# Kernel optimization log

Measured on AMD Instinct MI355X. Metric: run time of the kernel, lower is better.

Reference implementation:

```python
import jax, jax.numpy as jnp
import numpy as np

D_MODEL, D_STATE, D_CONV, EXPAND, DT_RANK = 1024, 16, 4, 2, 64
D_INNER = EXPAND * D_MODEL


def setup_inputs() -> dict:
    key = jax.random.key(0)
    ks = jax.random.split(key, 10)
    B, L = 2, 2048
    x = jax.random.normal(ks[0], (B, L, D_MODEL), dtype=jnp.float32)
    # torch nn.Linear weights are [out, in]; applied as x @ W.T
    in_proj_w = jax.random.normal(ks[1], (2 * D_INNER, D_MODEL), jnp.float32) * (D_MODEL ** -0.5)
    conv_w = jax.random.normal(ks[2], (D_INNER, 1, D_CONV), jnp.float32) * (D_CONV ** -0.5)
    conv_b = jax.random.normal(ks[3], (D_INNER,), jnp.float32) * 0.01
    x_proj_w = jax.random.normal(ks[4], (DT_RANK + 2 * D_STATE, D_INNER), jnp.float32) * (D_INNER ** -0.5)
    dt_init_std = DT_RANK ** -0.5
    dt_proj_w = jax.random.uniform(ks[5], (D_INNER, DT_RANK), jnp.float32, -dt_init_std, dt_init_std)
    # dt bias init: inverse-softplus of dt ~ LogUniform(1e-3, 1e-1)
    dt = jnp.exp(jax.random.uniform(ks[6], (D_INNER,), jnp.float32) * (np.log(0.1) - np.log(0.001)) + np.log(0.001))
    dt_proj_b = dt + jnp.log(-jnp.expm1(-dt))
    A_log = jnp.log(jnp.tile(jnp.arange(1, D_STATE + 1, dtype=jnp.float32), (D_INNER, 1)))  # [D_INNER, N]
    D_skip = jnp.ones((D_INNER,), jnp.float32)
    out_proj_w = jax.random.normal(ks[7], (D_MODEL, D_INNER), jnp.float32) * (D_INNER ** -0.5)
    return {"x": x, "in_proj_w": in_proj_w, "conv_w": conv_w, "conv_b": conv_b,
            "x_proj_w": x_proj_w, "dt_proj_w": dt_proj_w, "dt_proj_b": dt_proj_b,
            "A_log": A_log, "D_skip": D_skip, "out_proj_w": out_proj_w}


def selective_scan(u, delta, A, Bmat, Cmat, D_skip):
    # u, delta: [B, L, D]; A: [D, N]; Bmat, Cmat: [B, L, N]; D_skip: [D]
    def step(h, inp):
        delta_t, B_t, C_t, u_t = inp  # [B,D], [B,N], [B,N], [B,D]
        dA = jnp.exp(delta_t[..., None] * A)                      # [B,D,N]
        h = dA * h + (delta_t * u_t)[..., None] * B_t[:, None, :]  # [B,D,N]
        y_t = jnp.einsum('bdn,bn->bd', h, C_t)
        return h, y_t
    B_size, L, D_size = u.shape
    h0 = jnp.zeros((B_size, D_size, A.shape[-1]), u.dtype)
    xs = (jnp.swapaxes(delta, 0, 1), jnp.swapaxes(Bmat, 0, 1),
          jnp.swapaxes(Cmat, 0, 1), jnp.swapaxes(u, 0, 1))
    _, ys = jax.lax.scan(step, h0, xs)          # ys: [L, B, D]
    y = jnp.swapaxes(ys, 0, 1)                  # [B, L, D]
    return y + u * D_skip


def reference(x, in_proj_w, conv_w, conv_b, x_proj_w, dt_proj_w, dt_proj_b, A_log, D_skip, out_proj_w):
    B_size, L, _ = x.shape
    xz = x @ in_proj_w.T                         # [B, L, 2*D_INNER]
    x_ssm, z = jnp.split(xz, 2, axis=-1)
    # causal depthwise conv1d (torch pads d_conv-1 both sides then takes [:L])
    x_c = jnp.swapaxes(x_ssm, 1, 2)              # [B, D_INNER, L]
    x_c = jax.lax.conv_general_dilated(
        x_c, conv_w, window_strides=(1,), padding=[(D_CONV - 1, 0)],
        dimension_numbers=('NCH', 'OIH', 'NCH'), feature_group_count=D_INNER)
    x_c = x_c + conv_b[None, :, None]
    x_ssm = jax.nn.silu(jnp.swapaxes(x_c, 1, 2))  # [B, L, D_INNER]
    x_dbl = x_ssm @ x_proj_w.T                    # [B, L, dt_rank + 2N]
    dt, Bm, Cm = jnp.split(x_dbl, [DT_RANK, DT_RANK + D_STATE], axis=-1)
    delta = jax.nn.softplus(dt @ dt_proj_w.T + dt_proj_b)  # [B, L, D_INNER]
    A = -jnp.exp(A_log)                           # [D_INNER, N]
    y = selective_scan(x_ssm, delta, A, Bm, Cm, D_skip)
    y = y * jax.nn.silu(z)
    return y @ out_proj_w.T                       # [B, L, d_model]
```

## Files before the change

### kernel.cpp

```cpp
#include <hip/hip_runtime.h>
#include <hip/hip_bf16.h>
#include <math.h>

#define NB      2
#define LSEQ    2048
#define BLTOK   4096
#define DM      1024
#define DI      2048
#define NST     16
#define DTR     64
#define CH      64
#define LC      32

typedef __attribute__((ext_vector_type(8))) short short8;
typedef __attribute__((ext_vector_type(4))) float f32x4;

#define LDS_PTR(p) ((__attribute__((address_space(3))) void*)(p))
#define GLB_PTR(p) ((const __attribute__((address_space(1))) void*)(p))

static __device__ __forceinline__ unsigned short f2bf(float f) {
    unsigned int u = __float_as_uint(f);
    unsigned int r = (u + 0x7FFFu + ((u >> 16) & 1u)) >> 16;
    return (unsigned short)r;
}
static __device__ __forceinline__ float bf2f(unsigned short v) {
    return __uint_as_float((unsigned int)v << 16);
}

__launch_bounds__(256)
__global__ void cast_bf16(const float* __restrict__ in, unsigned short* __restrict__ out, int n4)
{
    int i = blockIdx.x * 256 + threadIdx.x;
    if (i < n4) {
        float4 v = ((const float4*)in)[i];
        uint2 o;
        o.x = (unsigned)f2bf(v.x) | ((unsigned)f2bf(v.y) << 16);
        o.y = (unsigned)f2bf(v.z) | ((unsigned)f2bf(v.w) << 16);
        ((uint2*)out)[i] = o;
    }
}

template<int EPI>
__launch_bounds__(256)
__global__ void gemm_db(const unsigned short* __restrict__ A,
                        const unsigned short* __restrict__ W,
                        void* __restrict__ Cout,
                        const float* __restrict__ bias,
                        int M, int N, int K, int lda, int ldb, int ldc)
{
    __shared__ unsigned short lds[2][2][128 * 64];

    const int tid = threadIdx.x;
    const int l = tid & 63;
    const int w = tid >> 6;
    const int wr = w >> 1, wc = w & 1;
    const int brow = blockIdx.y * 128;
    const int bcol = blockIdx.x * 128;

    const int strow = tid >> 3;
    const int scol  = ((tid & 7) ^ (strow & 7)) * 8;

    f32x4 acc[4][4];
#pragma unroll
    for (int i = 0; i < 4; ++i)
#pragma unroll
        for (int j = 0; j < 4; ++j) acc[i][j] = (f32x4)0.f;

    auto stage = [&](int bb, int k0) {
#pragma unroll
        for (int i = 0; i < 4; ++i) {
            const unsigned short* ga = A + (size_t)(brow + i * 32 + strow) * lda + k0 + scol;
            __builtin_amdgcn_global_load_lds(GLB_PTR(ga),
                LDS_PTR((char*)&lds[bb][0][0] + (i * 32 + w * 8) * 128), 16, 0, 0);
            const unsigned short* gb = W + (size_t)(bcol + i * 32 + strow) * ldb + k0 + scol;
            __builtin_amdgcn_global_load_lds(GLB_PTR(gb),
                LDS_PTR((char*)&lds[bb][1][0] + (i * 32 + w * 8) * 128), 16, 0, 0);
        }
    };

    auto compute = [&](int bb) {
        const char* baseA = (const char*)&lds[bb][0][0];
        const char* baseB = (const char*)&lds[bb][1][0];
        const int xo  = (l & 7) * 16;
        const int ko0 = (l >> 4) * 16;
#pragma unroll
        for (int ks = 0; ks < 2; ++ks) {
            const int kb = ks * 64 + ko0;
            short8 af[4], bfr[4];
#pragma unroll
            for (int i = 0; i < 4; ++i) {
                const int rowA = wr * 64 + i * 16 + (l & 15);
                af[i] = *(const short8*)(baseA + rowA * 128 + (kb ^ xo));
                const int rowB = wc * 64 + i * 16 + (l & 15);
                bfr[i] = *(const short8*)(baseB + rowB * 128 + (kb ^ xo));
            }
#pragma unroll
            for (int i = 0; i < 4; ++i)
#pragma unroll
                for (int j = 0; j < 4; ++j)
                    acc[i][j] = __builtin_amdgcn_mfma_f32_16x16x32_bf16(af[i], bfr[j], acc[i][j], 0, 0, 0);
        }
    };

    const int nt = K / 64;
    stage(0, 0);
    __syncthreads();
    int cur = 0;
    for (int t = 0; t < nt - 1; ++t) {
        stage(cur ^ 1, (t + 1) * 64);
        compute(cur);
        __syncthreads();
        cur ^= 1;
    }
    compute(cur);

#pragma unroll
    for (int i = 0; i < 4; ++i) {
        const int row0 = brow + wr * 64 + i * 16 + ((l >> 4) * 4);
#pragma unroll
        for (int j = 0; j < 4; ++j) {
            const int col = bcol + wc * 64 + j * 16 + (l & 15);
            if (EPI == 1) {
                unsigned short* Cb = (unsigned short*)Cout;
#pragma unroll
                for (int r = 0; r < 4; ++r)
                    Cb[(size_t)(row0 + r) * ldc + col] = f2bf(acc[i][j][r]);
            } else if (EPI == 2) {
                float* Cf = (float*)Cout;
                const float bv = bias[col];
#pragma unroll
                for (int r = 0; r < 4; ++r) {
                    float v = acc[i][j][r] + bv;
                    Cf[(size_t)(row0 + r) * ldc + col] = (v > 20.f) ? v : log1pf(__expf(v));
                }
            } else {
                float* Cf = (float*)Cout;
#pragma unroll
                for (int r = 0; r < 4; ++r)
                    Cf[(size_t)(row0 + r) * ldc + col] = acc[i][j][r];
            }
        }
    }
}

__launch_bounds__(256)
__global__ void gemm_mfma_sk(const unsigned short* __restrict__ A,
                             const unsigned short* __restrict__ W,
                             float* __restrict__ Cpart,
                             int M, int N, int K, int lda, int ldb, int ldc, int kslices)
{
    __shared__ unsigned short Asub[128 * 32];
    __shared__ unsigned short Bsub[128 * 32];

    const int tid = threadIdx.x;
    const int l = tid & 63;
    const int w = tid >> 6;
    const int wr = w >> 1, wc = w & 1;
    const int brow = blockIdx.y * 128;
    const int bcol = blockIdx.x * 128;
    const int ks = blockIdx.z;
    const int klen = K / kslices;
    const int kbeg = ks * klen;
    float* C = Cpart + (size_t)ks * M * ldc;

    f32x4 acc[4][4];
#pragma unroll
    for (int i = 0; i < 4; ++i)
#pragma unroll
        for (int j = 0; j < 4; ++j) acc[i][j] = (f32x4)0.f;

    const int srow = tid >> 2;
    const int scol = (tid & 3) * 8;

    for (int k0 = kbeg; k0 < kbeg + klen; k0 += 32) {
#pragma unroll
        for (int i = 0; i < 2; ++i) {
            const int ar = brow + i * 64 + srow;
            const unsigned short* ga = A + (size_t)ar * lda + k0 + scol;
            __builtin_amdgcn_global_load_lds(GLB_PTR(ga),
                LDS_PTR((char*)Asub + i * 4096 + w * 1024), 16, 0, 0);
            int nr = bcol + i * 64 + srow;
            if (nr > N - 1) nr = N - 1;
            const unsigned short* gb = W + (size_t)nr * ldb + k0 + scol;
            __builtin_amdgcn_global_load_lds(GLB_PTR(gb),
                LDS_PTR((char*)Bsub + i * 4096 + w * 1024), 16, 0, 0);
        }
        __syncthreads();

        short8 af[4], bf[4];
#pragma unroll
        for (int i = 0; i < 4; ++i) {
            const int row = wr * 64 + i * 16 + (l & 15);
            af[i] = *(const short8*)((const char*)Asub + row * 64 + (l >> 4) * 16);
        }
#pragma unroll
        for (int j = 0; j < 4; ++j) {
            const int row = wc * 64 + j * 16 + (l & 15);
            bf[j] = *(const short8*)((const char*)Bsub + row * 64 + (l >> 4) * 16);
        }
#pragma unroll
        for (int i = 0; i < 4; ++i)
#pragma unroll
            for (int j = 0; j < 4; ++j)
                acc[i][j] = __builtin_amdgcn_mfma_f32_16x16x32_bf16(af[i], bf[j], acc[i][j], 0, 0, 0);
        __syncthreads();
    }

#pragma unroll
    for (int i = 0; i < 4; ++i) {
        const int row0 = brow + wr * 64 + i * 16 + ((l >> 4) * 4);
#pragma unroll
        for (int j = 0; j < 4; ++j) {
            const int col = bcol + wc * 64 + j * 16 + (l & 15);
            if (col < N) {
#pragma unroll
                for (int r = 0; r < 4; ++r)
                    C[(size_t)(row0 + r) * ldc + col] = acc[i][j][r];
            }
        }
    }
}

__launch_bounds__(256)
__global__ void sk_reduce(const float* __restrict__ part, float* __restrict__ out,
                          unsigned short* __restrict__ dtb, int n4, int slices)
{
    int i = blockIdx.x * 256 + threadIdx.x;
    if (i < n4) {
        float4 s = ((const float4*)part)[i];
        for (int k = 1; k < slices; ++k) {
            float4 p = ((const float4*)part)[(size_t)k * n4 + i];
            s.x += p.x; s.y += p.y; s.z += p.z; s.w += p.w;
        }
        ((float4*)out)[i] = s;
        const int r = i / 24, cq = i % 24;
        if (cq < 16) {
            uint2 o;
            o.x = (unsigned)f2bf(s.x) | ((unsigned)f2bf(s.y) << 16);
            o.y = (unsigned)f2bf(s.z) | ((unsigned)f2bf(s.w) << 16);
            *(uint2*)&dtb[(size_t)r * DTR + cq * 4] = o;
        }
    }
}

__launch_bounds__(256)
__global__ void conv_silu_kernel(const unsigned short* __restrict__ xzb,
                                 const float* __restrict__ cw,
                                 const float* __restrict__ cb,
                                 unsigned short* __restrict__ ub)
{
    const int orig = blockIdx.x;
    const int bl = (orig & 7) * (BLTOK / 8) + (orig >> 3);
    const int l  = bl & (LSEQ - 1);
    const int d0 = threadIdx.x * 8;

    float acc[8];
    float4 w4[8];
#pragma unroll
    for (int q = 0; q < 8; ++q) {
        w4[q]  = *(const float4*)&cw[(d0 + q) * 4];
        acc[q] = cb[d0 + q];
    }
#pragma unroll
    for (int k = 0; k < 4; ++k) {
        const int ls = l - 3 + k;
        if (ls < 0) continue;
        short8 v = *(const short8*)&xzb[(size_t)(bl - 3 + k) * (2 * DI) + d0];
#pragma unroll
        for (int q = 0; q < 8; ++q) {
            const float wk = ((const float*)&w4[q])[k];
            acc[q] = fmaf(wk, bf2f((unsigned short)v[q]), acc[q]);
        }
    }
    short8 o;
#pragma unroll
    for (int q = 0; q < 8; ++q) {
        const float s = acc[q] / (1.f + __expf(-acc[q]));
        o[q] = (short)f2bf(s);
    }
    *(short8*)&ub[(size_t)bl * DI + d0] = o;
}

__launch_bounds__(256)
__global__ void scan_phase1(const float* __restrict__ delta, const unsigned short* __restrict__ ub,
                            const float* __restrict__ xdbl, const float* __restrict__ A_log,
                            float* __restrict__ P, float* __restrict__ S)
{
    __shared__ float s_d[8][256];
    __shared__ unsigned short s_u[8][256];
    __shared__ float sB[LC][NST];
    const int tid = threadIdx.x;
    const int d0 = blockIdx.x * 256;
    const int d  = d0 + tid;
    const int c = blockIdx.y;
    const int b = blockIdx.z;
    const int t0 = c * LC;

    for (int i = tid; i < LC * NST; i += 256)
        sB[i >> 4][i & 15] = xdbl[(size_t)(b * LSEQ + t0 + (i >> 4)) * 96 + 64 + (i & 15)];

    float Av[NST], Pv[NST], Sv[NST];
#pragma unroll
    for (int n = 0; n < NST; ++n) {
        Av[n] = -__expf(A_log[d * NST + n]) * 1.44269504f;
        Pv[n] = 1.f; Sv[n] = 0.f;
    }

    const float*          dbase = delta + (size_t)(b * LSEQ + t0) * DI + d0;
    const unsigned short* ubase = ub    + (size_t)(b * LSEQ + t0) * DI + d0;

    for (int sub = 0; sub < LC; sub += 8) {
        __syncthreads();
#pragma unroll
        for (int it = 0; it < 2; ++it) {
            const int slot = tid + it * 256;
            const int tt = slot >> 6, dq = (slot & 63) * 4;
            *(float4*)&s_d[tt][dq] = *(const float4*)(dbase + (size_t)(sub + tt) * DI + dq);
        }
        {
            const int tt = tid >> 5, d8 = (tid & 31) * 8;
            *(short8*)&s_u[tt][d8] = *(const short8*)(ubase + (size_t)(sub + tt) * DI + d8);
        }
        __syncthreads();
#pragma unroll
        for (int q = 0; q < 8; ++q) {
            const float dlt = s_d[q][tid];
            const float uu  = bf2f(s_u[q][tid]);
            const float du  = dlt * uu;
#pragma unroll
            for (int n = 0; n < NST; ++n) {
                const float dA = __builtin_amdgcn_exp2f(dlt * Av[n]);
                Pv[n] *= dA;
                Sv[n] = fmaf(dA, Sv[n], du * sB[sub + q][n]);
            }
        }
    }

    const size_t base = ((size_t)(b * CH + c) * DI + d) * NST;
#pragma unroll
    for (int n = 0; n < NST; n += 4) {
        *(f32x4*)&P[base + n] = (f32x4){Pv[n], Pv[n+1], Pv[n+2], Pv[n+3]};
        *(f32x4*)&S[base + n] = (f32x4){Sv[n], Sv[n+1], Sv[n+2], Sv[n+3]};
    }
}

__launch_bounds__(256)
__global__ void scan_phase2(const float* __restrict__ P, const float* __restrict__ S,
                            float* __restrict__ hin)
{
    const int g = blockIdx.x * 256 + threadIdx.x;
    const int n = g & 15;
    const int d = (g >> 4) & (DI - 1);
    const int b = g >> 15;
    float h = 0.f;
#pragma unroll 4
    for (int c = 0; c < CH; ++c) {
        const size_t idx = ((size_t)(b * CH + c) * DI + d) * NST + n;
        hin[idx] = h;
        h = fmaf(P[idx], h, S[idx]);
    }
}

__launch_bounds__(256)
__global__ void scan_phase3(const float* __restrict__ delta, const unsigned short* __restrict__ ub,
                            const float* __restrict__ xdbl, const float* __restrict__ A_log,
                            const float* __restrict__ Dskip, const unsigned short* __restrict__ xzb,
                            const float* __restrict__ hin, unsigned short* __restrict__ yg)
{
    __shared__ float s_d[8][256];
    __shared__ unsigned short s_u[8][256], s_z[8][256];
    __shared__ float sB[LC][NST], sC[LC][NST];
    const int tid = threadIdx.x;
    const int d0 = blockIdx.x * 256;
    const int d  = d0 + tid;
    const int c = blockIdx.y;
    const int b = blockIdx.z;
    const int t0 = c * LC;

    for (int i = tid; i < LC * NST; i += 256) {
        const size_t row = (size_t)(b * LSEQ + t0 + (i >> 4)) * 96;
        sB[i >> 4][i & 15] = xdbl[row + 64 + (i & 15)];
        sC[i >> 4][i & 15] = xdbl[row + 80 + (i & 15)];
    }

    float Av[NST], h[NST];
#pragma unroll
    for (int n = 0; n < NST; ++n)
        Av[n] = -__expf(A_log[d * NST + n]) * 1.44269504f;

    const size_t hbase = ((size_t)(b * CH + c) * DI + d) * NST;
#pragma unroll
    for (int n = 0; n < NST; n += 4) {
        f32x4 t = *(const f32x4*)&hin[hbase + n];
        h[n] = t.x; h[n+1] = t.y; h[n+2] = t.z; h[n+3] = t.w;
    }
    const float Dskv = Dskip[d];

    const float*          dbase = delta + (size_t)(b * LSEQ + t0) * DI + d0;
    const unsigned short* ubase = ub    + (size_t)(b * LSEQ + t0) * DI + d0;
    const unsigned short* zbase = xzb   + (size_t)(b * LSEQ + t0) * (2 * DI) + DI + d0;
    unsigned short* yrow = yg + (size_t)(b * LSEQ + t0) * DI + d;

    for (int sub = 0; sub < LC; sub += 8) {
        __syncthreads();
#pragma unroll
        for (int it = 0; it < 2; ++it) {
            const int slot = tid + it * 256;
            const int tt = slot >> 6, dq = (slot & 63) * 4;
            *(float4*)&s_d[tt][dq] = *(const float4*)(dbase + (size_t)(sub + tt) * DI + dq);
        }
        {
            const int tt = tid >> 5, d8 = (tid & 31) * 8;
            *(short8*)&s_u[tt][d8] = *(const short8*)(ubase + (size_t)(sub + tt) * DI + d8);
            *(short8*)&s_z[tt][d8] = *(const short8*)(zbase + (size_t)(sub + tt) * (2 * DI) + d8);
        }
        __syncthreads();
#pragma unroll
        for (int q = 0; q < 8; ++q) {
            const float dlt = s_d[q][tid];
            const float uu  = bf2f(s_u[q][tid]);
            const float du  = dlt * uu;
            float y = 0.f;
#pragma unroll
            for (int n = 0; n < NST; ++n) {
                const float dA = __builtin_amdgcn_exp2f(dlt * Av[n]);
                h[n] = fmaf(dA, h[n], du * sB[sub + q][n]);
                y = fmaf(h[n], sC[sub + q][n], y);
            }
            const float zv = bf2f(s_z[q][tid]);
            const float sig = __frcp_rn(1.f + __expf(-zv));
            const float val = (y + uu * Dskv) * (zv * sig);
            yrow[(size_t)(sub + q) * DI] = f2bf(val);
        }
    }
}

extern "C" void kernel_launch(void* const* d_in, const int* in_sizes, int n_in,
                              void* d_out, int out_size, void* d_ws, size_t ws_size,
                              hipStream_t stream)
{
    const float* x        = (const float*)d_in[0];
    const float* in_w     = (const float*)d_in[1];
    const float* conv_w   = (const float*)d_in[2];
    const float* conv_b   = (const float*)d_in[3];
    const float* xproj_w  = (const float*)d_in[4];
    const float* dtproj_w = (const float*)d_in[5];
    const float* dtproj_b = (const float*)d_in[6];
    const float* A_log    = (const float*)d_in[7];
    const float* Dskip    = (const float*)d_in[8];
    const float* out_w    = (const float*)d_in[9];
    float* out = (float*)d_out;

    char* ws = (char*)d_ws;
#define MB(x) ((size_t)(x) * 1024 * 1024)
    unsigned short* xzb   = (unsigned short*)(ws);
    unsigned short* ub    = (unsigned short*)(ws + MB(32));
    float*          delta = (float*)(ws + MB(48));
    float*          xdbl  = (float*)(ws + MB(80));
    unsigned short* ygb   = (unsigned short*)(ws + MB(82));
    float*          P     = (float*)(ws + MB(98));
    float*          S     = (float*)(ws + MB(114));
    float*          hin   = (float*)(ws + MB(130));
    unsigned short* xb    = (unsigned short*)(ws + MB(146));
    unsigned short* wb1   = (unsigned short*)(ws + MB(154));
    unsigned short* wb3   = (unsigned short*)(ws + MB(162));
    unsigned short* wb6   = (unsigned short*)(ws + MB(163));
    unsigned short* wb5   = (unsigned short*)(ws + MB(167));
    unsigned short* dtb   = (unsigned short*)(ws + MB(168));
    float*          xdbl_part = P;

    dim3 blk(256);

    cast_bf16<<<dim3((BLTOK * DM / 4 + 255) / 256), blk, 0, stream>>>(x, xb, BLTOK * DM / 4);
    cast_bf16<<<dim3((2 * DI * DM / 4 + 255) / 256), blk, 0, stream>>>(in_w, wb1, 2 * DI * DM / 4);
    cast_bf16<<<dim3((96 * DI / 4 + 255) / 256), blk, 0, stream>>>(xproj_w, wb3, 96 * DI / 4);
    cast_bf16<<<dim3((DM * DI / 4 + 255) / 256), blk, 0, stream>>>(out_w, wb6, DM * DI / 4);
    cast_bf16<<<dim3((DI * DTR / 4 + 255) / 256), blk, 0, stream>>>(dtproj_w, wb5, DI * DTR / 4);

    gemm_db<1><<<dim3(32, 32), blk, 0, stream>>>(xb, wb1, xzb, nullptr,
                                                 BLTOK, 2 * DI, DM, DM, DM, 2 * DI);

    conv_silu_kernel<<<dim3(BLTOK), blk, 0, stream>>>(xzb, conv_w, conv_b, ub);

    gemm_mfma_sk<<<dim3(1, 32, 8), blk, 0, stream>>>(ub, wb3, xdbl_part,
                                                     BLTOK, DTR + 2 * NST, DI, DI, DI, 96, 8);
    sk_reduce<<<dim3((BLTOK * 96 / 4 + 255) / 256), blk, 0, stream>>>(xdbl_part, xdbl, dtb,
                                                                      BLTOK * 96 / 4, 8);

    gemm_db<2><<<dim3(16, 32), blk, 0, stream>>>(dtb, wb5, delta, dtproj_b,
                                                 BLTOK, DI, DTR, DTR, DTR, DI);

    scan_phase1<<<dim3(DI / 256, CH, NB), blk, 0, stream>>>(delta, ub, xdbl, A_log, P, S);
    scan_phase2<<<dim3(NB * DI * NST / 256), blk, 0, stream>>>(P, S, hin);
    scan_phase3<<<dim3(DI / 256, CH, NB), blk, 0, stream>>>(delta, ub, xdbl, A_log, Dskip,
                                                            xzb, hin, ygb);

    gemm_db<0><<<dim3(8, 32), blk, 0, stream>>>(ygb, wb6, out, nullptr,
                                                BLTOK, DM, DI, DI, DI, DM);
}
```

Baseline: 263.4 us.

## Replace per-state exps with a power tree when A_log has integer-ratio structure

The scan phases check at runtime whether each channel's A values are integer multiples of the first one (A[n]=(n+1)*A0). When they are, one exp2 per timestep is computed and the other 15 decay factors come from a multiply tree. The chunk product P is now a single exp of the summed delta, which drops the running product. A general fallback path is kept for other inputs. The LDS staging of delta, u and z is replaced by direct per-thread global loads, and the chunk length is halved (CH=128, LC=16) with larger P/S/hin buffers. The trade-offs are more work in the sequential phase 2, more P/S traffic, and slightly different rounding from the repeated multiplies.

```diff
diff --git a/kernel.cpp b/kernel.cpp
--- a/kernel.cpp
+++ b/kernel.cpp
@@ -9,8 +9,9 @@
 #define DI      2048
 #define NST     16
 #define DTR     64
-#define CH      64
-#define LC      32
+#define CH      128
+#define LC      16
+#define LOG2E   1.44269504f
 
 typedef __attribute__((ext_vector_type(8))) short short8;
 typedef __attribute__((ext_vector_type(4))) float f32x4;
@@ -25,6 +26,25 @@
 }
 static __device__ __forceinline__ float bf2f(unsigned short v) {
     return __uint_as_float((unsigned int)v << 16);
+}
+
+static __device__ __forceinline__ void pow_tree(float w, float* e) {
+    e[0]  = w;
+    e[1]  = e[0] * e[0];
+    e[2]  = e[1] * e[0];
+    e[3]  = e[1] * e[1];
+    e[4]  = e[3] * e[0];
+    e[5]  = e[3] * e[1];
+    e[6]  = e[3] * e[2];
+    e[7]  = e[3] * e[3];
+    e[8]  = e[7] * e[0];
+    e[9]  = e[7] * e[1];
+    e[10] = e[7] * e[2];
+    e[11] = e[7] * e[3];
+    e[12] = e[7] * e[4];
+    e[13] = e[7] * e[5];
+    e[14] = e[7] * e[6];
+    e[15] = e[7] * e[7];
 }
 
 __launch_bounds__(256)
@@ -286,61 +306,77 @@
                             const float* __restrict__ xdbl, const float* __restrict__ A_log,
                             float* __restrict__ P, float* __restrict__ S)
 {
-    __shared__ float s_d[8][256];
-    __shared__ unsigned short s_u[8][256];
     __shared__ float sB[LC][NST];
     const int tid = threadIdx.x;
-    const int d0 = blockIdx.x * 256;
-    const int d  = d0 + tid;
+    const int d = blockIdx.x * 256 + tid;
     const int c = blockIdx.y;
     const int b = blockIdx.z;
     const int t0 = c * LC;
 
     for (int i = tid; i < LC * NST; i += 256)
         sB[i >> 4][i & 15] = xdbl[(size_t)(b * LSEQ + t0 + (i >> 4)) * 96 + 64 + (i & 15)];
-
-    float Av[NST], Pv[NST], Sv[NST];
-#pragma unroll
-    for (int n = 0; n < NST; ++n) {
-        Av[n] = -__expf(A_log[d * NST + n]) * 1.44269504f;
-        Pv[n] = 1.f; Sv[n] = 0.f;
-    }
-
-    const float*          dbase = delta + (size_t)(b * LSEQ + t0) * DI + d0;
-    const unsigned short* ubase = ub    + (size_t)(b * LSEQ + t0) * DI + d0;
-
-    for (int sub = 0; sub < LC; sub += 8) {
-        __syncthreads();
-#pragma unroll
-        for (int it = 0; it < 2; ++it) {
-            const int slot = tid + it * 256;
-            const int tt = slot >> 6, dq = (slot & 63) * 4;
-            *(float4*)&s_d[tt][dq] = *(const float4*)(dbase + (size_t)(sub + tt) * DI + dq);
-        }
-        {
-            const int tt = tid >> 5, d8 = (tid & 31) * 8;
-            *(short8*)&s_u[tt][d8] = *(const short8*)(ubase + (size_t)(sub + tt) * DI + d8);
-        }
-        __syncthreads();
-#pragma unroll
-        for (int q = 0; q < 8; ++q) {
-            const float dlt = s_d[q][tid];
-            const float uu  = bf2f(s_u[q][tid]);
+    __syncthreads();
+
+    const float Av0 = -__expf(A_log[d * NST]) * LOG2E;
+    bool fast = true;
+    for (int n = 1; n < NST; ++n) {
+        const float avn = -__expf(A_log[d * NST + n]) * LOG2E;
+        fast &= (fabsf(avn - (float)(n + 1) * Av0) <= 1e-3f * fabsf(avn));
+    }
+
+    float Sv[NST];
+    float dsum = 0.f;
+#pragma unroll
+    for (int n = 0; n < NST; ++n) Sv[n] = 0.f;
+
+    const float*          dbase = delta + (size_t)(b * LSEQ + t0) * DI + d;
+    const unsigned short* ubase = ub    + (size_t)(b * LSEQ + t0) * DI + d;
+
+    if (fast) {
+        for (int tg = 0; tg < LC; tg += 4) {
+            float dl[4], uu[4];
+#pragma unroll
+            for (int q = 0; q < 4; ++q) {
+                dl[q] = dbase[(size_t)(tg + q) * DI];
+                uu[q] = bf2f(ubase[(size_t)(tg + q) * DI]);
+            }
+#pragma unroll
+            for (int q = 0; q < 4; ++q) {
+                const float du = dl[q] * uu[q];
+                dsum += dl[q];
+                float e[NST];
+                pow_tree(__builtin_amdgcn_exp2f(dl[q] * Av0), e);
+#pragma unroll
+                for (int n = 0; n < NST; ++n)
+                    Sv[n] = fmaf(e[n], Sv[n], du * sB[tg + q][n]);
+            }
+        }
+        float Pv[NST];
+        pow_tree(__builtin_amdgcn_exp2f(dsum * Av0), Pv);
+        const size_t base = ((size_t)(b * CH + c) * DI + d) * NST;
+#pragma unroll
+        for (int n = 0; n < NST; n += 4) {
+            *(f32x4*)&P[base + n] = (f32x4){Pv[n], Pv[n+1], Pv[n+2], Pv[n+3]};
+            *(f32x4*)&S[base + n] = (f32x4){Sv[n], Sv[n+1], Sv[n+2], Sv[n+3]};
+        }
+    } else {
+        for (int t = 0; t < LC; ++t) {
+            const float dlt = dbase[(size_t)t * DI];
+            const float uu  = bf2f(ubase[(size_t)t * DI]);
             const float du  = dlt * uu;
-#pragma unroll
+            dsum += dlt;
             for (int n = 0; n < NST; ++n) {
-                const float dA = __builtin_amdgcn_exp2f(dlt * Av[n]);
-                Pv[n] *= dA;
-                Sv[n] = fmaf(dA, Sv[n], du * sB[sub + q][n]);
-            }
-        }
-    }
-
-    const size_t base = ((size_t)(b * CH + c) * DI + d) * NST;
-#pragma unroll
-    for (int n = 0; n < NST; n += 4) {
-        *(f32x4*)&P[base + n] = (f32x4){Pv[n], Pv[n+1], Pv[n+2], Pv[n+3]};
-        *(f32x4*)&S[base + n] = (f32x4){Sv[n], Sv[n+1], Sv[n+2], Sv[n+3]};
+                const float avn = -__expf(A_log[d * NST + n]) * LOG2E;
+                const float dA = __builtin_amdgcn_exp2f(dlt * avn);
+                Sv[n] = fmaf(dA, Sv[n], du * sB[t][n]);
+            }
+        }
+        const size_t base = ((size_t)(b * CH + c) * DI + d) * NST;
+        for (int n = 0; n < NST; ++n) {
+            const float avn = -__expf(A_log[d * NST + n]) * LOG2E;
+            P[base + n] = __builtin_amdgcn_exp2f(dsum * avn);
+            S[base + n] = Sv[n];
+        }
     }
 }
 
@@ -367,12 +403,9 @@
                             const float* __restrict__ Dskip, const unsigned short* __restrict__ xzb,
                             const float* __restrict__ hin, unsigned short* __restrict__ yg)
 {
-    __shared__ float s_d[8][256];
-    __shared__ unsigned short s_u[8][256], s_z[8][256];
     __shared__ float sB[LC][NST], sC[LC][NST];
     const int tid = threadIdx.x;
-    const int d0 = blockIdx.x * 256;
-    const int d  = d0 + tid;
+    const int d = blockIdx.x * 256 + tid;
     const int c = blockIdx.y;
     const int b = blockIdx.z;
     const int t0 = c * LC;
@@ -382,12 +415,16 @@
         sB[i >> 4][i & 15] = xdbl[row + 64 + (i & 15)];
         sC[i >> 4][i & 15] = xdbl[row + 80 + (i & 15)];
     }
-
-    float Av[NST], h[NST];
-#pragma unroll
-    for (int n = 0; n < NST; ++n)
-        Av[n] = -__expf(A_log[d * NST + n]) * 1.44269504f;
-
+    __syncthreads();
+
+    const float Av0 = -__expf(A_log[d * NST]) * LOG2E;
+    bool fast = true;
+    for (int n = 1; n < NST; ++n) {
+        const float avn = -__expf(A_log[d * NST + n]) * LOG2E;
+        fast &= (fabsf(avn - (float)(n + 1) * Av0) <= 1e-3f * fabsf(avn));
+    }
+
+    float h[NST];
     const size_t hbase = ((size_t)(b * CH + c) * DI + d) * NST;
 #pragma unroll
     for (int n = 0; n < NST; n += 4) {
@@ -396,41 +433,53 @@
     }
     const float Dskv = Dskip[d];
 
-    const float*          dbase = delta + (size_t)(b * LSEQ + t0) * DI + d0;
-    const unsigned short* ubase = ub    + (size_t)(b * LSEQ + t0) * DI + d0;
-    const unsigned short* zbase = xzb   + (size_t)(b * LSEQ + t0) * (2 * DI) + DI + d0;
+    const float*          dbase = delta + (size_t)(b * LSEQ + t0) * DI + d;
+    const unsigned short* ubase = ub    + (size_t)(b * LSEQ + t0) * DI + d;
+    const unsigned short* zbase = xzb   + (size_t)(b * LSEQ + t0) * (2 * DI) + DI + d;
     unsigned short* yrow = yg + (size_t)(b * LSEQ + t0) * DI + d;
 
-    for (int sub = 0; sub < LC; sub += 8) {
-        __syncthreads();
-#pragma unroll
-        for (int it = 0; it < 2; ++it) {
-            const int slot = tid + it * 256;
-            const int tt = slot >> 6, dq = (slot & 63) * 4;
-            *(float4*)&s_d[tt][dq] = *(const float4*)(dbase + (size_t)(sub + tt) * DI + dq);
-        }
-        {
-            const int tt = tid >> 5, d8 = (tid & 31) * 8;
-            *(short8*)&s_u[tt][d8] = *(const short8*)(ubase + (size_t)(sub + tt) * DI + d8);
-            *(short8*)&s_z[tt][d8] = *(const short8*)(zbase + (size_t)(sub + tt) * (2 * DI) + d8);
-        }
-        __syncthreads();
-#pragma unroll
-        for (int q = 0; q < 8; ++q) {
-            const float dlt = s_d[q][tid];
-            const float uu  = bf2f(s_u[q][tid]);
+    if (fast) {
+        for (int tg = 0; tg < LC; tg += 4) {
+            float dl[4], uu[4], zz[4];
+#pragma unroll
+            for (int q = 0; q < 4; ++q) {
+                dl[q] = dbase[(size_t)(tg + q) * DI];
+                uu[q] = bf2f(ubase[(size_t)(tg + q) * DI]);
+                zz[q] = bf2f(zbase[(size_t)(tg + q) * (2 * DI)]);
+            }
+#pragma unroll
+            for (int q = 0; q < 4; ++q) {
+                const float du = dl[q] * uu[q];
+                float e[NST];
+                pow_tree(__builtin_amdgcn_exp2f(dl[q] * Av0), e);
+                float y = 0.f;
+#pragma unroll
+                for (int n = 0; n < NST; ++n) {
+                    h[n] = fmaf(e[n], h[n], du * sB[tg + q][n]);
+                    y = fmaf(h[n], sC[tg + q][n], y);
+                }
+                const float zv = zz[q];
+                const float sig = __frcp_rn(1.f + __expf(-zv));
+                const float val = (y + uu[q] * Dskv) * (zv * sig);
+                yrow[(size_t)(tg + q) * DI] = f2bf(val);
+            }
+        }
+    } else {
+        for (int t = 0; t < LC; ++t) {
+            const float dlt = dbase[(size_t)t * DI];
+            const float uu  = bf2f(ubase[(size_t)t * DI]);
+            const float zv  = bf2f(zbase[(size_t)t * (2 * DI)]);
             const float du  = dlt * uu;
             float y = 0.f;
-#pragma unroll
             for (int n = 0; n < NST; ++n) {
-                const float dA = __builtin_amdgcn_exp2f(dlt * Av[n]);
-                h[n] = fmaf(dA, h[n], du * sB[sub + q][n]);
-                y = fmaf(h[n], sC[sub + q][n], y);
-            }
-            const float zv = bf2f(s_z[q][tid]);
+                const float avn = -__expf(A_log[d * NST + n]) * LOG2E;
+                const float dA = __builtin_amdgcn_exp2f(dlt * avn);
+                h[n] = fmaf(dA, h[n], du * sB[t][n]);
+                y = fmaf(h[n], sC[t][n], y);
+            }
             const float sig = __frcp_rn(1.f + __expf(-zv));
             const float val = (y + uu * Dskv) * (zv * sig);
-            yrow[(size_t)(sub + q) * DI] = f2bf(val);
+            yrow[(size_t)t * DI] = f2bf(val);
         }
     }
 }
@@ -459,14 +508,14 @@
     float*          xdbl  = (float*)(ws + MB(80));
     unsigned short* ygb   = (unsigned short*)(ws + MB(82));
     float*          P     = (float*)(ws + MB(98));
-    float*          S     = (float*)(ws + MB(114));
-    float*          hin   = (float*)(ws + MB(130));
-    unsigned short* xb    = (unsigned short*)(ws + MB(146));
-    unsigned short* wb1   = (unsigned short*)(ws + MB(154));
-    unsigned short* wb3   = (unsigned short*)(ws + MB(162));
-    unsigned short* wb6   = (unsigned short*)(ws + MB(163));
-    unsigned short* wb5   = (unsigned short*)(ws + MB(167));
-    unsigned short* dtb   = (unsigned short*)(ws + MB(168));
+    float*          S     = (float*)(ws + MB(130));
+    float*          hin   = (float*)(ws + MB(162));
+    unsigned short* xb    = (unsigned short*)(ws + MB(194));
+    unsigned short* wb1   = (unsigned short*)(ws + MB(202));
+    unsigned short* wb3   = (unsigned short*)(ws + MB(210));
+    unsigned short* wb6   = (unsigned short*)(ws + MB(211));
+    unsigned short* wb5   = (unsigned short*)(ws + MB(215));
+    unsigned short* dtb   = (unsigned short*)(ws + MB(216));
     float*          xdbl_part = P;
 
     dim3 blk(256);
```

Result: faster. 254.6 us (-3.3%).
